# Kernel optimization log

Hardware: AMD Instinct MI355X
Metric: run time of the kernel (lower is better)

Reference implementation:

```python
import jax, jax.numpy as jnp
import numpy as np

B, N, DIM = 8, 2048, 512
HEADS, DIM_HEAD = 8, 64
INNER = HEADS * DIM_HEAD  # 512
SCALE = DIM_HEAD ** -0.5
NEG = -1e9


def setup_inputs() -> dict:
    key = jax.random.key(0)
    ks = jax.random.split(key, 7)
    x = jax.random.normal(ks[0], (B, N, DIM), dtype=jnp.float32)
    adj = jax.random.uniform(ks[1], (B, N, N), dtype=jnp.float32)
    att_mask = jax.random.randint(ks[2], (B, 1, N, N), 0, 2).astype(jnp.bool_)
    W_gcn = jax.random.normal(ks[3], (DIM, DIM), dtype=jnp.float32) * (DIM ** -0.5)
    W_qkv = jax.random.normal(ks[4], (DIM, 3 * INNER), dtype=jnp.float32) * (DIM ** -0.5)
    W_out = jax.random.normal(ks[5], (INNER + DIM, DIM), dtype=jnp.float32) * ((INNER + DIM) ** -0.5)
    b_out = jax.random.normal(ks[6], (DIM,), dtype=jnp.float32) * 0.01
    return {"x": x, "adj": adj, "att_mask": att_mask,
            "W_gcn": W_gcn, "W_qkv": W_qkv, "W_out": W_out, "b_out": b_out}


def reference(x, adj, att_mask, W_gcn, W_qkv, W_out, b_out):
    # GCN branch: adj @ (x W_gcn)  -> [b, n, dim]
    gcn = jnp.einsum('bnj,bjd->bnd', adj, x @ W_gcn)

    # Attention branch
    qkv = x @ W_qkv                                  # [b, n, 3*inner]
    q, k, v = jnp.split(qkv, 3, axis=-1)
    split_heads = lambda t: t.reshape(B, N, HEADS, DIM_HEAD).transpose(0, 2, 1, 3)
    q, k, v = split_heads(q), split_heads(k), split_heads(v)  # [b, h, n, d]

    dots = jnp.einsum('bhid,bhjd->bhij', q, k) * SCALE        # [b, h, n, n]
    dots = jnp.where(att_mask, NEG, dots)
    attn = jax.nn.softmax(dots, axis=-1)
    att_out = jnp.einsum('bhij,bhjd->bhid', attn, v)          # [b, h, n, d]
    att_out = att_out.transpose(0, 2, 1, 3).reshape(B, N, INNER)

    out = jnp.concatenate([att_out, gcn], axis=-1)            # [b, n, inner+dim]
    return out @ W_out + b_out                                # [b, n, dim]
```

## Files before the change

kernel.cpp:

```cpp
#include <hip/hip_runtime.h>
#include <stdint.h>

#define DEVFN __device__ __forceinline__

typedef __attribute__((ext_vector_type(8))) short short8;
typedef __attribute__((ext_vector_type(4))) short short4v;
typedef __attribute__((ext_vector_type(4))) float floatx4;
typedef __attribute__((ext_vector_type(16))) float floatx16;
typedef __attribute__((ext_vector_type(4))) float vfloat4;
typedef __attribute__((ext_vector_type(2))) unsigned int uint2v;
typedef __attribute__((ext_vector_type(4))) unsigned int uint4v;

#define MFMA_BF16(a,b,c) __builtin_amdgcn_mfma_f32_16x16x32_bf16((a),(b),(c),0,0,0)
#define MFMA32_BF16(a,b,c) __builtin_amdgcn_mfma_f32_32x32x16_bf16((a),(b),(c),0,0,0)
#define GL2LDS(g,l) __builtin_amdgcn_global_load_lds((const __attribute__((address_space(1))) void*)(g), (__attribute__((address_space(3))) void*)(l), 16, 0, 0)

DEVFN unsigned short f2bf(float f){
  unsigned u = __float_as_uint(f);
  u = (u + 0x7fffu + ((u >> 16) & 1u)) >> 16;
  return (unsigned short)u;
}

DEVFN unsigned cvtpk_bf16(float lo, float hi){
  unsigned r;
  asm("v_cvt_pk_bf16_f32 %0, %1, %2" : "=v"(r) : "v"(lo), "v"(hi));
  return r;
}

__global__ void detect_kernel(const unsigned char* m, unsigned int* flag){
  if (threadIdx.x == 0) *flag = 0u;
  __syncthreads();
  int any = 0;
  for (int i = threadIdx.x; i < 4096; i += 256)
    if ((i & 3) != 0 && m[i]) any = 1;
  if (any) atomicOr(flag, 1u);
}

__global__ void prep_kernel(const float* __restrict__ x, const float* __restrict__ wg,
                            const float* __restrict__ wq, const float* __restrict__ wo,
                            const void* __restrict__ mask, const unsigned* __restrict__ flag,
                            const float* __restrict__ adj,
                            unsigned short* __restrict__ xbf, unsigned short* __restrict__ wcat,
                            unsigned short* __restrict__ woutT, unsigned* __restrict__ mp,
                            unsigned short* __restrict__ adjb)
{
  int bid = blockIdx.x, tid = threadIdx.x;
  if (bid < 8192) {
    int i = (bid*256 + tid)*4;
    vfloat4 v = *(const vfloat4*)&x[i];
    short4v c; c[0]=(short)f2bf(v[0]); c[1]=(short)f2bf(v[1]); c[2]=(short)f2bf(v[2]); c[3]=(short)f2bf(v[3]);
    *(short4v*)&xbf[i] = c;
  } else if (bid < 8192 + 4096) {
    int i = (bid - 8192)*256 + tid;
    int k = i & 511, c = i >> 9;
    float v = (c < 512) ? wg[k*512 + c] : wq[k*1536 + (c - 512)];
    wcat[c*512 + k] = (unsigned short)f2bf(v);
  } else if (bid < 8192 + 4096 + 2048) {
    int i = (bid - 12288)*256 + tid;
    int k = i & 1023, n2 = i >> 10;
    woutT[n2*1024 + k] = (unsigned short)f2bf(wo[k*512 + n2]);
  } else if (bid < 145408) {
    int j = bid - 14336;
    int e = j*256 + tid;
    int v;
    if (*flag) v = ((const unsigned char*)mask)[e];
    else       v = ((const int*)mask)[e];
    unsigned long long ball = __ballot(v != 0);
    int base = e & ~63;
    int lane = tid & 63;
    if (lane == 0)  mp[(base >> 5) + 0] = (unsigned)(ball & 0xffffffffull);
    if (lane == 32) mp[(base >> 5) + 1] = (unsigned)(ball >> 32);
  } else {
    int i = ((bid - 145408)*256 + tid)*4;
    vfloat4 v = *(const vfloat4*)&adj[i];
    short4v c; c[0]=(short)f2bf(v[0]); c[1]=(short)f2bf(v[1]); c[2]=(short)f2bf(v[2]); c[3]=(short)f2bf(v[3]);
    *(short4v*)&adjb[i] = c;
  }
}

DEVFN void gemm_kloop_bf16(const unsigned short* Ag, int lda,
                           const unsigned short* Bg, int ldb, int K,
                           short* As, short* Bs, int w, int l,
                           floatx4 (&acc)[4][4])
{
  const int wr = (w >> 1)*64, wc = (w & 1)*64;
  for (int k0 = 0; k0 < K; k0 += 32) {
    __syncthreads();
#pragma unroll
    for (int i = 0; i < 2; i++) {
      int id = (w*2 + i)*64 + l;
      int row = id >> 2, part = id & 3;
      GL2LDS(Ag + row*lda + k0 + part*8, As + (w*2 + i)*512);
      GL2LDS(Bg + row*ldb + k0 + part*8, Bs + (w*2 + i)*512);
    }
    __syncthreads();
    short8 af[4], bfr[4];
#pragma unroll
    for (int t = 0; t < 4; t++) {
      af[t]  = *(const short8*)&As[(wr + t*16 + (l & 15))*32 + ((l >> 4) << 3)];
      bfr[t] = *(const short8*)&Bs[(wc + t*16 + (l & 15))*32 + ((l >> 4) << 3)];
    }
#pragma unroll
    for (int a2 = 0; a2 < 4; a2++)
#pragma unroll
      for (int b2 = 0; b2 < 4; b2++)
        acc[a2][b2] = MFMA_BF16(af[a2], bfr[b2], acc[a2][b2]);
  }
}

__global__ __launch_bounds__(256, 2)
void gemm_ab_kernel(const unsigned short* __restrict__ xbf, const unsigned short* __restrict__ wcat,
                    unsigned short* __restrict__ xgT, unsigned short* __restrict__ Qo,
                    unsigned short* __restrict__ Ko, unsigned short* __restrict__ VTo)
{
  __shared__ short lds[16384];
  int tid = threadIdx.x, w = tid >> 6, l = tid & 63;
  int bid = blockIdx.x;
  int xcd = bid & 7, slot = bid >> 3;
  int p  = xcd + ((slot >> 4) << 3);
  int nt = slot & 15;
  int rows0 = p*128, cols0 = nt*128;

  floatx4 acc[4][4];
  const floatx4 zf = {0.f, 0.f, 0.f, 0.f};
#pragma unroll
  for (int a2 = 0; a2 < 4; a2++)
#pragma unroll
    for (int b2 = 0; b2 < 4; b2++) acc[a2][b2] = zf;

  gemm_kloop_bf16(xbf + rows0*512, 512, wcat + cols0*512, 512, 512,
                  lds, lds + 4096, w, l, acc);
  __syncthreads();

  int wr = (w >> 1)*64, wc = (w & 1)*64;
  int b = p >> 4;
  int n0 = (p & 15)*128 + wr;
  int gc0 = cols0 + wc;

  if (nt < 4 || nt >= 12) {
    short* T = lds + w*4096;
#pragma unroll
    for (int mi = 0; mi < 4; mi++)
#pragma unroll
      for (int bi = 0; bi < 4; bi++)
#pragma unroll
        for (int r = 0; r < 4; r++) {
          int rl = mi*16 + ((l >> 4) << 2) + r;
          int cl = bi*16 + (l & 15);
          T[cl*64 + ((((rl >> 3) ^ (cl & 7))) << 3) + (rl & 7)] = (short)f2bf(acc[mi][bi][r]);
        }
#pragma unroll
    for (int i = 0; i < 8; i++) {
      int chunk = i*64 + l;
      int c = chunk >> 3, s = chunk & 7;
      short8 v = *(const short8*)&T[c*64 + ((s ^ (c & 7)) << 3)];
      int rowstart = n0 + s*8;
      if (nt < 4) {
        int d = gc0 + c;
        *(short8*)&xgT[(b*512 + d)*2048 + rowstart] = v;
      } else {
        int vc = gc0 + c - 1536;
        int hh = vc >> 6, dd = vc & 63;
        *(short8*)&VTo[((b*8 + hh)*64 + dd)*2048 + rowstart] = v;
      }
    }
  } else {
    unsigned short* dst = (nt < 8) ? Qo : Ko;
    int cbase = gc0 - ((nt < 8) ? 512 : 1024);
    int hh = cbase >> 6;
#pragma unroll
    for (int mi = 0; mi < 4; mi++)
#pragma unroll
      for (int bi = 0; bi < 4; bi++)
#pragma unroll
        for (int r = 0; r < 4; r++) {
          int rowg = n0 + mi*16 + ((l >> 4) << 2) + r;
          int dd = bi*16 + (l & 15);
          dst[((b*8 + hh)*2048 + rowg)*64 + dd] = (unsigned short)f2bf(acc[mi][bi][r]);
        }
  }
}

__global__ __launch_bounds__(256, 2)
void gemm_c_bf16_kernel(const unsigned short* __restrict__ adjb, const unsigned short* __restrict__ xgT,
                        unsigned short* __restrict__ cat)
{
  __shared__ short lds[8192];
  int tid = threadIdx.x, w = tid >> 6, l = tid & 63;
  int bid = blockIdx.x;
  int xcd = bid & 7, slot = bid >> 3;
  int p  = xcd + ((slot >> 2) << 3);
  int nt = slot & 3;
  int b = p >> 4, mt = p & 15;
  int rows0 = mt*128, cols0 = nt*128;

  floatx4 acc[4][4];
  const floatx4 zf = {0.f, 0.f, 0.f, 0.f};
#pragma unroll
  for (int a2 = 0; a2 < 4; a2++)
#pragma unroll
    for (int b2 = 0; b2 < 4; b2++) acc[a2][b2] = zf;

  gemm_kloop_bf16(adjb + (size_t)b*2048*2048 + (size_t)rows0*2048, 2048,
                  xgT + (b*512 + cols0)*2048, 2048, 2048,
                  lds, lds + 4096, w, l, acc);

  int wr = (w >> 1)*64, wc = (w & 1)*64;
#pragma unroll
  for (int mi = 0; mi < 4; mi++)
#pragma unroll
    for (int bi = 0; bi < 4; bi++)
#pragma unroll
      for (int r = 0; r < 4; r++) {
        int rowg = b*2048 + rows0 + wr + mi*16 + ((l >> 4) << 2) + r;
        int col  = 512 + cols0 + wc + bi*16 + (l & 15);
        cat[rowg*1024 + col] = (unsigned short)f2bf(acc[mi][bi][r]);
      }
}

__global__ __launch_bounds__(256, 2)
void gemm_c_f32_kernel(const float* __restrict__ adj, const unsigned short* __restrict__ xgT,
                       unsigned short* __restrict__ cat)
{
  __shared__ short lds[8192];
  int tid = threadIdx.x, w = tid >> 6, l = tid & 63;
  int bid = blockIdx.x;
  int xcd = bid & 7, slot = bid >> 3;
  int p  = xcd + ((slot >> 2) << 3);
  int nt = slot & 3;
  int b = p >> 4, mt = p & 15;
  int rows0 = mt*128, cols0 = nt*128;
  const float* Ag = adj + (size_t)b*2048*2048 + (size_t)rows0*2048;
  const unsigned short* Bg = xgT + (b*512 + cols0)*2048;

  floatx4 acc[4][4];
  const floatx4 zf = {0.f, 0.f, 0.f, 0.f};
#pragma unroll
  for (int a2 = 0; a2 < 4; a2++)
#pragma unroll
    for (int b2 = 0; b2 < 4; b2++) acc[a2][b2] = zf;

  const int wr = (w >> 1)*64, wc = (w & 1)*64;
  for (int k0 = 0; k0 < 2048; k0 += 32) {
    __syncthreads();
#pragma unroll
    for (int i = 0; i < 4; i++) {
      int id = (w*4 + i)*64 + l;
      int row = id >> 3, part = id & 7;
      vfloat4 v = *(const vfloat4*)&Ag[row*2048 + k0 + part*4];
      short4v c4; c4[0]=(short)f2bf(v[0]); c4[1]=(short)f2bf(v[1]); c4[2]=(short)f2bf(v[2]); c4[3]=(short)f2bf(v[3]);
      *(short4v*)&lds[row*32 + part*4] = c4;
    }
#pragma unroll
    for (int i = 0; i < 2; i++) {
      int id = (w*2 + i)*64 + l;
      int row = id >> 2, part = id & 3;
      GL2LDS(Bg + row*2048 + k0 + part*8, lds + 4096 + (w*2 + i)*512);
    }
    __syncthreads();
    short8 af[4], bfr[4];
#pragma unroll
    for (int t = 0; t < 4; t++) {
      af[t]  = *(const short8*)&lds[(wr + t*16 + (l & 15))*32 + ((l >> 4) << 3)];
      bfr[t] = *(const short8*)&lds[4096 + (wc + t*16 + (l & 15))*32 + ((l >> 4) << 3)];
    }
#pragma unroll
    for (int a2 = 0; a2 < 4; a2++)
#pragma unroll
      for (int b2 = 0; b2 < 4; b2++)
        acc[a2][b2] = MFMA_BF16(af[a2], bfr[b2], acc[a2][b2]);
  }

#pragma unroll
  for (int mi = 0; mi < 4; mi++)
#pragma unroll
    for (int bi = 0; bi < 4; bi++)
#pragma unroll
      for (int r = 0; r < 4; r++) {
        int rowg = b*2048 + rows0 + wr + mi*16 + ((l >> 4) << 2) + r;
        int col  = 512 + cols0 + wc + bi*16 + (l & 15);
        cat[rowg*1024 + col] = (unsigned short)f2bf(acc[mi][bi][r]);
      }
}

DEVFN void attn_stage(const unsigned short* KB, const unsigned short* VB,
                      short* Ks, short* Vs, int kn0, int w, int l)
{
#pragma unroll
  for (int i = 0; i < 2; i++) {
    int id = (w*2 + i)*64 + l;
    int row = id >> 3, sl = id & 7;
    int sp = sl ^ (row & 7);
    GL2LDS(KB + (kn0 + row)*64 + sp*8, Ks + (w*2 + i)*512);
    GL2LDS(VB + row*2048 + kn0 + sp*8, Vs + (w*2 + i)*512);
  }
}

__global__ __launch_bounds__(256, 4)
void attn_kernel(const unsigned short* __restrict__ Q, const unsigned short* __restrict__ Kb,
                 const unsigned short* __restrict__ VT, const unsigned* __restrict__ mp,
                 unsigned short* __restrict__ cat)
{
  __shared__ short lds[16384];
  int tid = threadIdx.x, w = tid >> 6, l = tid & 63;
  int c5 = l & 31, h = l >> 5;
  int hv = h*4;
  int paddr = (l ^ 32) << 2;

  int bid = blockIdx.x;
  int xcd = bid & 7, slot = bid >> 3;
  int bh = xcd + ((slot >> 4) << 3);
  int qt = slot & 15;
  int b = bh >> 3, hd = bh & 7;
  int qw = qt*128 + w*32;

  const unsigned short* Qb = Q  + (size_t)bh*2048*64;
  const unsigned short* KB = Kb + (size_t)bh*2048*64;
  const unsigned short* VB = VT + (size_t)bh*64*2048;
  const unsigned* mrow = mp + b*2048*64 + (qw + c5)*64;

  short8 qf[4];
#pragma unroll
  for (int dk = 0; dk < 4; dk++)
    qf[dk] = *(const short8*)&Qb[(qw + c5)*64 + dk*16 + h*8];

  floatx16 oacc[2];
  const floatx16 zf16 = {0.f,0.f,0.f,0.f,0.f,0.f,0.f,0.f,0.f,0.f,0.f,0.f,0.f,0.f,0.f,0.f};
  oacc[0] = zf16; oacc[1] = zf16;
  float dsum = 0.f;

  const float C_SL2E = 0.125f * 1.44269504f;

  attn_stage(KB, VB, lds, lds + 8192, 0, w, l);
  asm volatile("s_waitcnt vmcnt(0)" ::: "memory");
  __builtin_amdgcn_s_barrier();
  asm volatile("" ::: "memory");

  for (int kt = 0; kt < 32; kt++) {
    int cur = kt & 1;
    short* Ks = lds + cur*4096;
    short* Vs = lds + 8192 + cur*4096;

    if (kt < 31)
      attn_stage(KB, VB, lds + (cur ^ 1)*4096, lds + 8192 + (cur ^ 1)*4096, kt*64 + 64, w, l);

    uint2v wd = *(const uint2v*)&mrow[kt*2];

#pragma unroll
    for (int kb = 0; kb < 2; kb++) {
      floatx16 sacc = zf16;
      __builtin_amdgcn_s_setprio(1);
#pragma unroll
      for (int dk = 0; dk < 4; dk++) {
        int row = kb*32 + c5;
        int sl = dk*2 + h;
        short8 kf = *(const short8*)&Ks[row*64 + ((sl ^ (row & 7)) << 3)];
        sacc = MFMA32_BF16(kf, qf[dk], sacc);
      }
      __builtin_amdgcn_s_setprio(0);

      unsigned wsh = (kb ? wd.y : wd.x) >> hv;
      float ps[16];
#pragma unroll
      for (int t = 0; t < 16; t++) {
        int bit = (wsh >> ((t >> 2)*8 + (t & 3))) & 1;
        float p = exp2f(sacc[t] * C_SL2E);
        p = bit ? 0.f : p;
        dsum += p;
        ps[t] = p;
      }
      unsigned pk[4][2];
#pragma unroll
      for (int s = 0; s < 4; s++) {
        pk[s][0] = cvtpk_bf16(ps[s*4 + 0], ps[s*4 + 1]);
        pk[s][1] = cvtpk_bf16(ps[s*4 + 2], ps[s*4 + 3]);
      }

#pragma unroll
      for (int ksl = 0; ksl < 2; ksl++) {
        unsigned own0 = h ? pk[2*ksl + 1][0] : pk[2*ksl][0];
        unsigned own1 = h ? pk[2*ksl + 1][1] : pk[2*ksl][1];
        unsigned snd0 = h ? pk[2*ksl][0]     : pk[2*ksl + 1][0];
        unsigned snd1 = h ? pk[2*ksl][1]     : pk[2*ksl + 1][1];
        unsigned prm0 = (unsigned)__builtin_amdgcn_ds_bpermute(paddr, (int)snd0);
        unsigned prm1 = (unsigned)__builtin_amdgcn_ds_bpermute(paddr, (int)snd1);
        uint4v fu;
        fu[0] = h ? prm0 : own0;
        fu[1] = h ? prm1 : own1;
        fu[2] = h ? own0 : prm0;
        fu[3] = h ? own1 : prm1;
        short8 pfrag = *(short8*)&fu;

        __builtin_amdgcn_s_setprio(1);
#pragma unroll
        for (int db = 0; db < 2; db++) {
          int row = db*32 + c5;
          int sl = kb*4 + ksl*2 + h;
          short8 vf = *(const short8*)&Vs[row*64 + ((sl ^ (row & 7)) << 3)];
          oacc[db] = MFMA32_BF16(pfrag, vf, oacc[db]);
        }
        __builtin_amdgcn_s_setprio(0);
      }
    }

    asm volatile("s_waitcnt vmcnt(0)" ::: "memory");
    __builtin_amdgcn_s_barrier();
    asm volatile("" ::: "memory");
  }

  dsum += __shfl_xor(dsum, 32);
  float inv = 1.0f / dsum;

#pragma unroll
  for (int db = 0; db < 2; db++)
#pragma unroll
    for (int t = 0; t < 16; t++) {
      int qrow = qw + (t & 3) + 8*(t >> 2) + hv;
      int col = hd*64 + db*32 + c5;
      cat[(b*2048 + qrow)*1024 + col] = (unsigned short)f2bf(oacc[db][t] * inv);
    }
}

__global__ __launch_bounds__(256, 2)
void gemm_d_kernel(const unsigned short* __restrict__ cat, const unsigned short* __restrict__ woutT,
                   const float* __restrict__ bout, float* __restrict__ out)
{
  __shared__ short lds[8192];
  int tid = threadIdx.x, w = tid >> 6, l = tid & 63;
  int bid = blockIdx.x;
  int xcd = bid & 7, slot = bid >> 3;
  int p  = xcd + ((slot >> 2) << 3);
  int nt = slot & 3;
  int rows0 = p*128, cols0 = nt*128;

  floatx4 acc[4][4];
  const floatx4 zf = {0.f, 0.f, 0.f, 0.f};
#pragma unroll
  for (int a2 = 0; a2 < 4; a2++)
#pragma unroll
    for (int b2 = 0; b2 < 4; b2++) acc[a2][b2] = zf;

  gemm_kloop_bf16(cat + (size_t)rows0*1024, 1024, woutT + cols0*1024, 1024, 1024,
                  lds, lds + 4096, w, l, acc);

  int wr = (w >> 1)*64, wc = (w & 1)*64;
#pragma unroll
  for (int bi = 0; bi < 4; bi++) {
    int col = cols0 + wc + bi*16 + (l & 15);
    float bias = bout[col];
#pragma unroll
    for (int mi = 0; mi < 4; mi++)
#pragma unroll
      for (int r = 0; r < 4; r++) {
        int rowg = rows0 + wr + mi*16 + ((l >> 4) << 2) + r;
        out[rowg*512 + col] = acc[mi][bi][r] + bias;
      }
  }
}

extern "C" void kernel_launch(void* const* d_in, const int* in_sizes, int n_in,
                              void* d_out, int out_size, void* d_ws, size_t ws_size,
                              hipStream_t stream)
{
  (void)in_sizes; (void)n_in; (void)out_size;
  const float* x   = (const float*)d_in[0];
  const float* adj = (const float*)d_in[1];
  const void*  msk = d_in[2];
  const float* wg  = (const float*)d_in[3];
  const float* wq  = (const float*)d_in[4];
  const float* wo  = (const float*)d_in[5];
  const float* bo  = (const float*)d_in[6];
  float* out = (float*)d_out;
  char* ws = (char*)d_ws;

  unsigned short* xbf   = (unsigned short*)(ws + 0);
  unsigned short* wcat  = (unsigned short*)(ws + 16777216);
  unsigned short* woutT = (unsigned short*)(ws + 18874368);
  unsigned short* xgT   = (unsigned short*)(ws + 19922944);
  unsigned short* Qb    = (unsigned short*)(ws + 36700160);
  unsigned short* Kb    = (unsigned short*)(ws + 53477376);
  unsigned short* VTb   = (unsigned short*)(ws + 70254592);
  unsigned short* cat   = (unsigned short*)(ws + 87031808);
  unsigned*       mp    = (unsigned*)(ws + 120586240);
  unsigned*       flag  = (unsigned*)(ws + 124780544);
  unsigned short* adjb  = (unsigned short*)(ws + 124780608);

  const int use_adjb = (ws_size >= (size_t)124780608 + 67108864) ? 1 : 0;

  detect_kernel<<<1, 256, 0, stream>>>((const unsigned char*)msk, flag);
  prep_kernel<<<use_adjb ? 178176 : 145408, 256, 0, stream>>>(
      x, wg, wq, wo, msk, flag, adj, xbf, wcat, woutT, mp, adjb);
  gemm_ab_kernel<<<2048, 256, 0, stream>>>(xbf, wcat, xgT, Qb, Kb, VTb);
  if (use_adjb)
    gemm_c_bf16_kernel<<<512, 256, 0, stream>>>(adjb, xgT, cat);
  else
    gemm_c_f32_kernel<<<512, 256, 0, stream>>>(adj, xgT, cat);
  attn_kernel<<<1024, 256, 0, stream>>>(Qb, Kb, VTb, mp, cat);
  gemm_d_kernel<<<512, 256, 0, stream>>>(cat, woutT, bo, out);
}
```

Measured before the change: 395.0 us.

## Load V fragments directly from global and compute row sums via MFMA

Result: slower. 433.4 us (+9.7%).

```diff
diff --git a/kernel.cpp b/kernel.cpp
--- a/kernel.cpp
+++ b/kernel.cpp
@@ -283,16 +283,14 @@
       }
 }
 
-DEVFN void attn_stage(const unsigned short* KB, const unsigned short* VB,
-                      short* Ks, short* Vs, int kn0, int w, int l)
+DEVFN void attn_stage_k(const unsigned short* KB, short* buf, int kn0, int w, int l)
 {
 #pragma unroll
   for (int i = 0; i < 2; i++) {
     int id = (w*2 + i)*64 + l;
     int row = id >> 3, sl = id & 7;
     int sp = sl ^ (row & 7);
-    GL2LDS(KB + (kn0 + row)*64 + sp*8, Ks + (w*2 + i)*512);
-    GL2LDS(VB + row*2048 + kn0 + sp*8, Vs + (w*2 + i)*512);
+    GL2LDS(KB + (kn0 + row)*64 + sp*8, buf + (w*2 + i)*512);
   }
 }
 
@@ -301,7 +299,7 @@
                  const unsigned short* __restrict__ VT, const unsigned* __restrict__ mp,
                  unsigned short* __restrict__ cat)
 {
-  __shared__ short lds[16384];
+  __shared__ short lds[8192];
   int tid = threadIdx.x, w = tid >> 6, l = tid & 63;
   int c5 = l & 31, h = l >> 5;
   int hv = h*4;
@@ -318,20 +316,23 @@
   const unsigned short* KB = Kb + (size_t)bh*2048*64;
   const unsigned short* VB = VT + (size_t)bh*64*2048;
   const unsigned* mrow = mp + b*2048*64 + (qw + c5)*64;
+  const unsigned short* vrow0 = VB + c5*2048 + h*8;
+  const unsigned short* vrow1 = VB + (32 + c5)*2048 + h*8;
 
   short8 qf[4];
 #pragma unroll
   for (int dk = 0; dk < 4; dk++)
     qf[dk] = *(const short8*)&Qb[(qw + c5)*64 + dk*16 + h*8];
 
-  floatx16 oacc[2];
+  floatx16 oacc0, oacc1, nacc;
   const floatx16 zf16 = {0.f,0.f,0.f,0.f,0.f,0.f,0.f,0.f,0.f,0.f,0.f,0.f,0.f,0.f,0.f,0.f};
-  oacc[0] = zf16; oacc[1] = zf16;
-  float dsum = 0.f;
-
+  oacc0 = zf16; oacc1 = zf16; nacc = zf16;
+
+  const short8 ones8 = {(short)0x3F80,(short)0x3F80,(short)0x3F80,(short)0x3F80,
+                        (short)0x3F80,(short)0x3F80,(short)0x3F80,(short)0x3F80};
   const float C_SL2E = 0.125f * 1.44269504f;
 
-  attn_stage(KB, VB, lds, lds + 8192, 0, w, l);
+  attn_stage_k(KB, lds, 0, w, l);
   asm volatile("s_waitcnt vmcnt(0)" ::: "memory");
   __builtin_amdgcn_s_barrier();
   asm volatile("" ::: "memory");
@@ -339,15 +340,21 @@
   for (int kt = 0; kt < 32; kt++) {
     int cur = kt & 1;
     short* Ks = lds + cur*4096;
-    short* Vs = lds + 8192 + cur*4096;
 
     if (kt < 31)
-      attn_stage(KB, VB, lds + (cur ^ 1)*4096, lds + 8192 + (cur ^ 1)*4096, kt*64 + 64, w, l);
+      attn_stage_k(KB, lds + (cur ^ 1)*4096, kt*64 + 64, w, l);
 
     uint2v wd = *(const uint2v*)&mrow[kt*2];
 
 #pragma unroll
     for (int kb = 0; kb < 2; kb++) {
+      short8 vga[2], vgb[2];
+#pragma unroll
+      for (int ksl = 0; ksl < 2; ksl++) {
+        vga[ksl] = *(const short8*)&vrow0[kt*64 + (kb*2 + ksl)*16];
+        vgb[ksl] = *(const short8*)&vrow1[kt*64 + (kb*2 + ksl)*16];
+      }
+
       floatx16 sacc = zf16;
       __builtin_amdgcn_s_setprio(1);
 #pragma unroll
@@ -366,7 +373,6 @@
         int bit = (wsh >> ((t >> 2)*8 + (t & 3))) & 1;
         float p = exp2f(sacc[t] * C_SL2E);
         p = bit ? 0.f : p;
-        dsum += p;
         ps[t] = p;
       }
       unsigned pk[4][2];
@@ -392,13 +398,9 @@
         short8 pfrag = *(short8*)&fu;
 
         __builtin_amdgcn_s_setprio(1);
-#pragma unroll
-        for (int db = 0; db < 2; db++) {
-          int row = db*32 + c5;
-          int sl = kb*4 + ksl*2 + h;
-          short8 vf = *(const short8*)&Vs[row*64 + ((sl ^ (row & 7)) << 3)];
-          oacc[db] = MFMA32_BF16(pfrag, vf, oacc[db]);
-        }
+        oacc0 = MFMA32_BF16(pfrag, vga[ksl], oacc0);
+        oacc1 = MFMA32_BF16(pfrag, vgb[ksl], oacc1);
+        nacc  = MFMA32_BF16(pfrag, ones8, nacc);
         __builtin_amdgcn_s_setprio(0);
       }
     }
@@ -408,17 +410,14 @@
     asm volatile("" ::: "memory");
   }
 
-  dsum += __shfl_xor(dsum, 32);
-  float inv = 1.0f / dsum;
-
-#pragma unroll
-  for (int db = 0; db < 2; db++)
-#pragma unroll
-    for (int t = 0; t < 16; t++) {
-      int qrow = qw + (t & 3) + 8*(t >> 2) + hv;
-      int col = hd*64 + db*32 + c5;
-      cat[(b*2048 + qrow)*1024 + col] = (unsigned short)f2bf(oacc[db][t] * inv);
-    }
+#pragma unroll
+  for (int t = 0; t < 16; t++) {
+    float iv = 1.0f / nacc[t];
+    int qrow = qw + (t & 3) + 8*(t >> 2) + hv;
+    unsigned short* orow = &cat[(b*2048 + qrow)*1024 + hd*64];
+    orow[c5]      = (unsigned short)f2bf(oacc0[t] * iv);
+    orow[32 + c5] = (unsigned short)f2bf(oacc1[t] * iv);
+  }
 }
 
 __global__ __launch_bounds__(256, 2)
```

## Compute softmax denominator via MFMA with ones vector and reswizzle K/V LDS

Applied to the files above, without the earlier changes.

Result: no change. 394.4 us (-0.2%).

```diff
diff --git a/kernel.cpp b/kernel.cpp
--- a/kernel.cpp
+++ b/kernel.cpp
@@ -290,7 +290,7 @@
   for (int i = 0; i < 2; i++) {
     int id = (w*2 + i)*64 + l;
     int row = id >> 3, sl = id & 7;
-    int sp = sl ^ (row & 7);
+    int sp = sl ^ (row & 7) ^ (((row >> 3) & 3) << 1);
     GL2LDS(KB + (kn0 + row)*64 + sp*8, Ks + (w*2 + i)*512);
     GL2LDS(VB + row*2048 + kn0 + sp*8, Vs + (w*2 + i)*512);
   }
@@ -324,11 +324,12 @@
   for (int dk = 0; dk < 4; dk++)
     qf[dk] = *(const short8*)&Qb[(qw + c5)*64 + dk*16 + h*8];
 
-  floatx16 oacc[2];
+  floatx16 oacc0, oacc1, nacc;
   const floatx16 zf16 = {0.f,0.f,0.f,0.f,0.f,0.f,0.f,0.f,0.f,0.f,0.f,0.f,0.f,0.f,0.f,0.f};
-  oacc[0] = zf16; oacc[1] = zf16;
-  float dsum = 0.f;
-
+  oacc0 = zf16; oacc1 = zf16; nacc = zf16;
+
+  const short8 ones8 = {(short)0x3F80,(short)0x3F80,(short)0x3F80,(short)0x3F80,
+                        (short)0x3F80,(short)0x3F80,(short)0x3F80,(short)0x3F80};
   const float C_SL2E = 0.125f * 1.44269504f;
 
   attn_stage(KB, VB, lds, lds + 8192, 0, w, l);
@@ -354,7 +355,8 @@
       for (int dk = 0; dk < 4; dk++) {
         int row = kb*32 + c5;
         int sl = dk*2 + h;
-        short8 kf = *(const short8*)&Ks[row*64 + ((sl ^ (row & 7)) << 3)];
+        int sw = sl ^ (row & 7) ^ (((row >> 3) & 3) << 1);
+        short8 kf = *(const short8*)&Ks[row*64 + (sw << 3)];
         sacc = MFMA32_BF16(kf, qf[dk], sacc);
       }
       __builtin_amdgcn_s_setprio(0);
@@ -366,7 +368,6 @@
         int bit = (wsh >> ((t >> 2)*8 + (t & 3))) & 1;
         float p = exp2f(sacc[t] * C_SL2E);
         p = bit ? 0.f : p;
-        dsum += p;
         ps[t] = p;
       }
       unsigned pk[4][2];
@@ -396,9 +397,12 @@
         for (int db = 0; db < 2; db++) {
           int row = db*32 + c5;
           int sl = kb*4 + ksl*2 + h;
-          short8 vf = *(const short8*)&Vs[row*64 + ((sl ^ (row & 7)) << 3)];
-          oacc[db] = MFMA32_BF16(pfrag, vf, oacc[db]);
+          int sw = sl ^ (row & 7) ^ (((row >> 3) & 3) << 1);
+          short8 vf = *(const short8*)&Vs[row*64 + (sw << 3)];
+          if (db == 0) oacc0 = MFMA32_BF16(pfrag, vf, oacc0);
+          else         oacc1 = MFMA32_BF16(pfrag, vf, oacc1);
         }
+        nacc = MFMA32_BF16(pfrag, ones8, nacc);
         __builtin_amdgcn_s_setprio(0);
       }
     }
@@ -408,17 +412,14 @@
     asm volatile("" ::: "memory");
   }
 
-  dsum += __shfl_xor(dsum, 32);
-  float inv = 1.0f / dsum;
-
-#pragma unroll
-  for (int db = 0; db < 2; db++)
-#pragma unroll
-    for (int t = 0; t < 16; t++) {
-      int qrow = qw + (t & 3) + 8*(t >> 2) + hv;
-      int col = hd*64 + db*32 + c5;
-      cat[(b*2048 + qrow)*1024 + col] = (unsigned short)f2bf(oacc[db][t] * inv);
-    }
+#pragma unroll
+  for (int t = 0; t < 16; t++) {
+    float iv = 1.0f / nacc[t];
+    int qrow = qw + (t & 3) + 8*(t >> 2) + hv;
+    unsigned short* orow = &cat[(b*2048 + qrow)*1024 + hd*64];
+    orow[c5]      = (unsigned short)f2bf(oacc0[t] * iv);
+    orow[32 + c5] = (unsigned short)f2bf(oacc1[t] * iv);
+  }
 }
 
 __global__ __launch_bounds__(256, 2)
```
